# Kernel tuning notes

Measured on AMD Instinct MI355X. Metric: run time of the kernel, lower is better.

Reference implementation:

```python
import jax, jax.numpy as jnp
import numpy as np

EPS = 1e-12  # torch F.normalize default eps


def _l2_normalize(x):
    # normalize along last dim, matching F.normalize(dim=2)
    norm = jnp.linalg.norm(x, axis=-1, keepdims=True)
    return x / jnp.maximum(norm, EPS)


def _poly_kernel_mean(a, b):
    # mean over (B,C,C) of squared inner products along T.
    # Original does broadcast (B,1,C,T)*(B,C,1,T) then sum; einsum is the
    # efficient batched-matmul form of the same math.
    g = jnp.einsum('bct,bdt->bcd', a, b)  # (B,C,C)
    return jnp.mean(g * g)


def setup_inputs() -> dict:
    key = jax.random.key(0)
    k1, k2 = jax.random.split(key)
    B, C, T = 16, 128, 16384
    f_s = jax.random.normal(k1, (B, C, T), dtype=jnp.float32)
    f_t = jax.random.normal(k2, (B, C, T), dtype=jnp.float32)
    return {"f_s": f_s, "f_t": f_t}


def reference(f_s, f_t):
    # equal T -> no interpolation branch; view(B,C,-1) is identity for 3D
    s = _l2_normalize(f_s)
    t = _l2_normalize(f_t)
    loss = (jax.lax.stop_gradient(_poly_kernel_mean(t, t))
            + _poly_kernel_mean(s, s)
            - 2.0 * _poly_kernel_mean(s, t))
    return loss
```

## Files before the change

### kernel.cpp

```cpp
#include <hip/hip_runtime.h>
#include <hip/hip_bf16.h>

#define BATCH  16
#define CCH    128
#define TDIM   16384
#define MROWS  256
#define NCHUNK 16
#define KC     (TDIM / NCHUNK)
#define BK     32
#define NSTEP  (KC / BK)
#define LDSP   40
#define GRAM   (MROWS * MROWS)

typedef __attribute__((ext_vector_type(8))) short bf16x8;
typedef __attribute__((ext_vector_type(4))) float f32x4;
typedef __attribute__((ext_vector_type(4))) unsigned short u16x4;

__device__ __forceinline__ unsigned short f2bf(float x) {
  unsigned int u = __float_as_uint(x);
  u += 0x7fffu + ((u >> 16) & 1u);
  return (unsigned short)(u >> 16);
}

__global__ __launch_bounds__(512, 2) void gram_kernel(
    const float* __restrict__ fs, const float* __restrict__ ft,
    float* __restrict__ outp, int atomic_mode)
{
  __shared__ __attribute__((aligned(16))) unsigned short sm[2][MROWS][LDSP];

  const int tid   = threadIdx.x;
  const int bidx  = blockIdx.x;
  const int b     = bidx / NCHUNK;
  const int chunk = bidx - b * NCHUNK;
  const int kbase = chunk * KC;

  const int lane = tid & 63;
  const int w    = tid >> 6;
  const int wr   = w & 3;
  const int wc   = w >> 2;
  const int lhi  = lane >> 4;
  const int llo  = lane & 15;
  const int koff = lhi * 8;

  const float* rowptr[4];
  int rowidx[4], kq4[4];
  #pragma unroll
  for (int j = 0; j < 4; ++j) {
    int idx = j * 512 + tid;
    int row = idx >> 3;
    int kq  = idx & 7;
    rowidx[j] = row;
    kq4[j]    = kq * 4;
    const float* base = (row < CCH)
        ? (fs + (size_t)(b * CCH + row) * TDIM)
        : (ft + (size_t)(b * CCH + (row - CCH)) * TDIM);
    rowptr[j] = base + kbase + kq * 4;
  }

  f32x4 acc[4][8];
  #pragma unroll
  for (int i = 0; i < 4; ++i)
    #pragma unroll
    for (int j = 0; j < 8; ++j)
      acc[i][j] = (f32x4){0.f, 0.f, 0.f, 0.f};

  #pragma unroll
  for (int j = 0; j < 4; ++j) {
    f32x4 v = *(const f32x4*)(rowptr[j]);
    u16x4 p;
    p.x = f2bf(v.x); p.y = f2bf(v.y); p.z = f2bf(v.z); p.w = f2bf(v.w);
    *(u16x4*)&sm[0][rowidx[j]][kq4[j]] = p;
  }
  __syncthreads();

  int cur = 0;
  #pragma unroll 1
  for (int s = 0; s < NSTEP - 1; ++s) {
    f32x4 v[4];
    #pragma unroll
    for (int j = 0; j < 4; ++j)
      v[j] = *(const f32x4*)(rowptr[j] + (s + 1) * BK);

    bf16x8 af[4], bfr[8];
    #pragma unroll
    for (int i = 0; i < 4; ++i)
      af[i] = *(const bf16x8*)&sm[cur][wr * 64 + i * 16 + llo][koff];
    #pragma unroll
    for (int j = 0; j < 8; ++j)
      bfr[j] = *(const bf16x8*)&sm[cur][wc * 128 + j * 16 + llo][koff];
    #pragma unroll
    for (int i = 0; i < 4; ++i)
      #pragma unroll
      for (int j = 0; j < 8; ++j)
        acc[i][j] = __builtin_amdgcn_mfma_f32_16x16x32_bf16(af[i], bfr[j], acc[i][j], 0, 0, 0);

    #pragma unroll
    for (int j = 0; j < 4; ++j) {
      u16x4 p;
      p.x = f2bf(v[j].x); p.y = f2bf(v[j].y); p.z = f2bf(v[j].z); p.w = f2bf(v[j].w);
      *(u16x4*)&sm[cur ^ 1][rowidx[j]][kq4[j]] = p;
    }
    __syncthreads();
    cur ^= 1;
  }

  {
    bf16x8 af[4], bfr[8];
    #pragma unroll
    for (int i = 0; i < 4; ++i)
      af[i] = *(const bf16x8*)&sm[cur][wr * 64 + i * 16 + llo][koff];
    #pragma unroll
    for (int j = 0; j < 8; ++j)
      bfr[j] = *(const bf16x8*)&sm[cur][wc * 128 + j * 16 + llo][koff];
    #pragma unroll
    for (int i = 0; i < 4; ++i)
      #pragma unroll
      for (int j = 0; j < 8; ++j)
        acc[i][j] = __builtin_amdgcn_mfma_f32_16x16x32_bf16(af[i], bfr[j], acc[i][j], 0, 0, 0);
  }

  if (atomic_mode) {
    float* out = outp + (size_t)b * GRAM;
    #pragma unroll
    for (int i = 0; i < 4; ++i) {
      int row0 = wr * 64 + i * 16 + lhi * 4;
      #pragma unroll
      for (int j = 0; j < 8; ++j) {
        int col = wc * 128 + j * 16 + llo;
        #pragma unroll
        for (int r = 0; r < 4; ++r)
          atomicAdd(&out[(size_t)(row0 + r) * MROWS + col], acc[i][j][r]);
      }
    }
  } else {
    float* out = outp + (size_t)bidx * GRAM;
    #pragma unroll
    for (int i = 0; i < 4; ++i) {
      int row0 = wr * 64 + i * 16 + lhi * 4;
      #pragma unroll
      for (int j = 0; j < 8; ++j) {
        int col = wc * 128 + j * 16 + llo;
        #pragma unroll
        for (int r = 0; r < 4; ++r)
          out[(size_t)(row0 + r) * MROWS + col] = acc[i][j][r];
      }
    }
  }
}

__global__ __launch_bounds__(256) void norms_kernel(
    const float* __restrict__ gram, float* __restrict__ norms, int nchunk)
{
  int b = blockIdx.x;
  int d = threadIdx.x;
  float g = 0.f;
  for (int c = 0; c < nchunk; ++c)
    g += gram[(size_t)(b * nchunk + c) * GRAM + (size_t)d * (MROWS + 1)];
  float n = sqrtf(fmaxf(g, 0.f));
  n = fmaxf(n, 1e-12f);
  norms[b * MROWS + d] = 1.0f / n;
}

__global__ __launch_bounds__(256) void loss_kernel(
    const float* __restrict__ gram, const float* __restrict__ norms,
    float* __restrict__ out, int nchunk)
{
  int b     = blockIdx.x >> 6;
  int strip = blockIdx.x & 63;
  int e0    = strip * 1024 + threadIdx.x * 4;
  const float* nb = norms + b * MROWS;

  f32x4 g = (f32x4){0.f, 0.f, 0.f, 0.f};
  for (int c = 0; c < nchunk; ++c) {
    f32x4 v = *(const f32x4*)(gram + (size_t)(b * nchunk + c) * GRAM + e0);
    g.x += v.x; g.y += v.y; g.z += v.z; g.w += v.w;
  }
  int i  = e0 >> 8;
  int j0 = e0 & 255;
  float ri = nb[i];
  float accl = 0.f;
  #pragma unroll
  for (int q = 0; q < 4; ++q) {
    int j = j0 + q;
    float gh = g[q] * ri * nb[j];
    float sgn = ((i < CCH) == (j < CCH)) ? 1.f : -1.f;
    accl += sgn * gh * gh;
  }
  #pragma unroll
  for (int off = 32; off > 0; off >>= 1)
    accl += __shfl_down(accl, off, 64);
  __shared__ float red[4];
  if ((threadIdx.x & 63) == 0) red[threadIdx.x >> 6] = accl;
  __syncthreads();
  if (threadIdx.x == 0) {
    float t = red[0] + red[1] + red[2] + red[3];
    atomicAdd(out, t * (1.0f / (float)(BATCH * CCH * CCH)));
  }
}

extern "C" void kernel_launch(void* const* d_in, const int* in_sizes, int n_in,
                              void* d_out, int out_size, void* d_ws, size_t ws_size,
                              hipStream_t stream) {
  const float* fs = (const float*)d_in[0];
  const float* ft = (const float*)d_in[1];
  float* out = (float*)d_out;
  float* wsf = (float*)d_ws;

  float* norms = wsf;
  float* gram  = wsf + 4096;

  const size_t need_partials = (size_t)(4096 + (size_t)BATCH * NCHUNK * GRAM) * 4;
  const int atomic_mode = (ws_size >= need_partials) ? 0 : 1;
  const int nchunk = atomic_mode ? 1 : NCHUNK;

  (void)hipMemsetAsync(d_out, 0, sizeof(float), stream);
  if (atomic_mode)
    (void)hipMemsetAsync(gram, 0, (size_t)BATCH * GRAM * sizeof(float), stream);

  gram_kernel<<<dim3(BATCH * NCHUNK), dim3(512), 0, stream>>>(fs, ft, gram, atomic_mode);
  norms_kernel<<<dim3(BATCH), dim3(256), 0, stream>>>(gram, norms, nchunk);
  loss_kernel<<<dim3(BATCH * 64), dim3(256), 0, stream>>>(gram, norms, out, nchunk);
}
```

Before: 349.3 us.

## Deepen global-load prefetch to two steps and use lighter LDS barrier

Restructures the gram kernel main loop so global loads are issued two K-steps ahead with two register buffers, unrolled by two over the double-buffered LDS. The __syncthreads is replaced by an LDS-only waitcnt plus s_barrier, so outstanding global loads are not drained at each barrier. This is meant to hide HBM latency better, at the cost of extra live registers (a second f32x4[4] set) that could raise register pressure at 2 blocks per CU.

```diff
diff --git a/kernel.cpp b/kernel.cpp
--- a/kernel.cpp
+++ b/kernel.cpp
@@ -22,6 +22,50 @@
   return (unsigned short)(u >> 16);
 }
 
+__device__ __forceinline__ void pipe_barrier() {
+  asm volatile("s_waitcnt lgkmcnt(0)" ::: "memory");
+  __builtin_amdgcn_s_barrier();
+  asm volatile("" ::: "memory");
+}
+
+__device__ __forceinline__ void load_step(
+    f32x4 (&v)[4], const float* const (&rowptr)[4], int s)
+{
+  #pragma unroll
+  for (int j = 0; j < 4; ++j)
+    v[j] = *(const f32x4*)(rowptr[j] + s * BK);
+}
+
+__device__ __forceinline__ void stage_step(
+    unsigned short (&buf)[MROWS][LDSP], const f32x4 (&v)[4],
+    const int (&rowidx)[4], const int (&kq4)[4])
+{
+  #pragma unroll
+  for (int j = 0; j < 4; ++j) {
+    u16x4 p;
+    p.x = f2bf(v[j].x); p.y = f2bf(v[j].y); p.z = f2bf(v[j].z); p.w = f2bf(v[j].w);
+    *(u16x4*)&buf[rowidx[j]][kq4[j]] = p;
+  }
+}
+
+__device__ __forceinline__ void compute_step(
+    const unsigned short (&buf)[MROWS][LDSP],
+    f32x4 (&acc)[4][8], int wr, int wc, int llo, int koff)
+{
+  bf16x8 af[4], bfr[8];
+  #pragma unroll
+  for (int i = 0; i < 4; ++i)
+    af[i] = *(const bf16x8*)&buf[wr * 64 + i * 16 + llo][koff];
+  #pragma unroll
+  for (int j = 0; j < 8; ++j)
+    bfr[j] = *(const bf16x8*)&buf[wc * 128 + j * 16 + llo][koff];
+  #pragma unroll
+  for (int i = 0; i < 4; ++i)
+    #pragma unroll
+    for (int j = 0; j < 8; ++j)
+      acc[i][j] = __builtin_amdgcn_mfma_f32_16x16x32_bf16(af[i], bfr[j], acc[i][j], 0, 0, 0);
+}
+
 __global__ __launch_bounds__(512, 2) void gram_kernel(
     const float* __restrict__ fs, const float* __restrict__ ft,
     float* __restrict__ outp, int atomic_mode)
@@ -64,60 +108,27 @@
     for (int j = 0; j < 8; ++j)
       acc[i][j] = (f32x4){0.f, 0.f, 0.f, 0.f};
 
-  #pragma unroll
-  for (int j = 0; j < 4; ++j) {
-    f32x4 v = *(const f32x4*)(rowptr[j]);
-    u16x4 p;
-    p.x = f2bf(v.x); p.y = f2bf(v.y); p.z = f2bf(v.z); p.w = f2bf(v.w);
-    *(u16x4*)&sm[0][rowidx[j]][kq4[j]] = p;
-  }
-  __syncthreads();
-
-  int cur = 0;
+  f32x4 va[4], vb[4];
+  load_step(va, rowptr, 0);
+  load_step(vb, rowptr, 1);
+  stage_step(sm[0], va, rowidx, kq4);
+  pipe_barrier();
+
   #pragma unroll 1
-  for (int s = 0; s < NSTEP - 1; ++s) {
-    f32x4 v[4];
-    #pragma unroll
-    for (int j = 0; j < 4; ++j)
-      v[j] = *(const f32x4*)(rowptr[j] + (s + 1) * BK);
-
-    bf16x8 af[4], bfr[8];
-    #pragma unroll
-    for (int i = 0; i < 4; ++i)
-      af[i] = *(const bf16x8*)&sm[cur][wr * 64 + i * 16 + llo][koff];
-    #pragma unroll
-    for (int j = 0; j < 8; ++j)
-      bfr[j] = *(const bf16x8*)&sm[cur][wc * 128 + j * 16 + llo][koff];
-    #pragma unroll
-    for (int i = 0; i < 4; ++i)
-      #pragma unroll
-      for (int j = 0; j < 8; ++j)
-        acc[i][j] = __builtin_amdgcn_mfma_f32_16x16x32_bf16(af[i], bfr[j], acc[i][j], 0, 0, 0);
-
-    #pragma unroll
-    for (int j = 0; j < 4; ++j) {
-      u16x4 p;
-      p.x = f2bf(v[j].x); p.y = f2bf(v[j].y); p.z = f2bf(v[j].z); p.w = f2bf(v[j].w);
-      *(u16x4*)&sm[cur ^ 1][rowidx[j]][kq4[j]] = p;
-    }
-    __syncthreads();
-    cur ^= 1;
-  }
-
-  {
-    bf16x8 af[4], bfr[8];
-    #pragma unroll
-    for (int i = 0; i < 4; ++i)
-      af[i] = *(const bf16x8*)&sm[cur][wr * 64 + i * 16 + llo][koff];
-    #pragma unroll
-    for (int j = 0; j < 8; ++j)
-      bfr[j] = *(const bf16x8*)&sm[cur][wc * 128 + j * 16 + llo][koff];
-    #pragma unroll
-    for (int i = 0; i < 4; ++i)
-      #pragma unroll
-      for (int j = 0; j < 8; ++j)
-        acc[i][j] = __builtin_amdgcn_mfma_f32_16x16x32_bf16(af[i], bfr[j], acc[i][j], 0, 0, 0);
-  }
+  for (int s = 0; s < NSTEP - 2; s += 2) {
+    load_step(va, rowptr, s + 2);
+    compute_step(sm[0], acc, wr, wc, llo, koff);
+    stage_step(sm[1], vb, rowidx, kq4);
+    pipe_barrier();
+    load_step(vb, rowptr, s + 3);
+    compute_step(sm[1], acc, wr, wc, llo, koff);
+    stage_step(sm[0], va, rowidx, kq4);
+    pipe_barrier();
+  }
+  compute_step(sm[0], acc, wr, wc, llo, koff);
+  stage_step(sm[1], vb, rowidx, kq4);
+  pipe_barrier();
+  compute_step(sm[1], acc, wr, wc, llo, koff);
 
   if (atomic_mode) {
     float* out = outp + (size_t)b * GRAM;
```

After: 332.6 us. -4.8%, faster.

## Pre-pack inputs to swizzled bf16 and stream into LDS via global_load_lds

Applied to the files above, without the earlier changes.

Adds a pack kernel that converts both fp32 inputs to bf16 in a chunked, XOR-swizzled layout. The gram kernel then copies those tiles straight into 128KB of dynamic LDS with global_load_lds, double-buffered over larger K steps, and drops the per-step fp32 load and convert in the main loop. Partial grams are always reduced with atomics instead of per-chunk partial buffers. This costs an extra pass that writes and rereads a bf16 copy of the inputs, and adds atomic contention on the output.

```diff
diff --git a/kernel.cpp b/kernel.cpp
--- a/kernel.cpp
+++ b/kernel.cpp
@@ -1,20 +1,23 @@
 #include <hip/hip_runtime.h>
-#include <hip/hip_bf16.h>
 
 #define BATCH  16
 #define CCH    128
 #define TDIM   16384
 #define MROWS  256
 #define NCHUNK 16
-#define KC     (TDIM / NCHUNK)
-#define BK     32
-#define NSTEP  (KC / BK)
-#define LDSP   40
+#define KC     1024
+#define BKS    128
+#define NSTEP  8
+#define STEPB  65536u
+#define REGSH  262144u
+#define LDSBYTES (2u * STEPB)
 #define GRAM   (MROWS * MROWS)
 
 typedef __attribute__((ext_vector_type(8))) short bf16x8;
 typedef __attribute__((ext_vector_type(4))) float f32x4;
-typedef __attribute__((ext_vector_type(4))) unsigned short u16x4;
+typedef __attribute__((ext_vector_type(8))) unsigned short u16x8;
+typedef const __attribute__((address_space(1))) unsigned int* gptr_t;
+typedef __attribute__((address_space(3))) unsigned int* lptr_t;
 
 __device__ __forceinline__ unsigned short f2bf(float x) {
   unsigned int u = __float_as_uint(x);
@@ -22,17 +25,67 @@
   return (unsigned short)(u >> 16);
 }
 
+__global__ __launch_bounds__(256) void pack_kernel(
+    const float* __restrict__ fs, const float* __restrict__ ft,
+    unsigned short* __restrict__ pk)
+{
+  const int id  = blockIdx.x;
+  const int tau = id >> 11;
+  const int b   = (id >> 7) & 15;
+  const int row = id & 127;
+  const int R   = tau * CCH + row;
+  const int r7  = R & 7;
+  const float* src = (tau ? ft : fs) + (size_t)(b * CCH + row) * TDIM;
+  unsigned short* dstb = pk + (size_t)b * NCHUNK * REGSH + (size_t)R * 128;
+
+  #pragma unroll 1
+  for (int it = 0; it < 8; ++it) {
+    const int k = it * 2048 + threadIdx.x * 8;
+    f32x4 lo = *(const f32x4*)(src + k);
+    f32x4 hi = *(const f32x4*)(src + k + 4);
+    u16x8 p;
+    p[0] = f2bf(lo.x); p[1] = f2bf(lo.y); p[2] = f2bf(lo.z); p[3] = f2bf(lo.w);
+    p[4] = f2bf(hi.x); p[5] = f2bf(hi.y); p[6] = f2bf(hi.z); p[7] = f2bf(hi.w);
+    const int c  = k >> 10;
+    const int s  = (k >> 7) & 7;
+    const int cl = (k >> 3) & 15;
+    unsigned short* dst = dstb + (size_t)c * REGSH + (unsigned)s * 32768u
+                        + (unsigned)((cl ^ r7) << 3);
+    *(u16x8*)dst = p;
+  }
+}
+
+__device__ __forceinline__ void compute_kk(
+    const unsigned short* bp, f32x4 (&acc)[4][8], int kk,
+    int wr, int wc, int llo, int lhi)
+{
+  bf16x8 af[4], bfr[8];
+  #pragma unroll
+  for (int i = 0; i < 4; ++i) {
+    const int R = wr * 64 + i * 16 + llo;
+    af[i] = *(const bf16x8*)(bp + R * 128 + (((kk * 4 + lhi) ^ (R & 7)) << 3));
+  }
+  #pragma unroll
+  for (int j = 0; j < 8; ++j) {
+    const int R = wc * 128 + j * 16 + llo;
+    bfr[j] = *(const bf16x8*)(bp + R * 128 + (((kk * 4 + lhi) ^ (R & 7)) << 3));
+  }
+  #pragma unroll
+  for (int i = 0; i < 4; ++i)
+    #pragma unroll
+    for (int j = 0; j < 8; ++j)
+      acc[i][j] = __builtin_amdgcn_mfma_f32_16x16x32_bf16(af[i], bfr[j], acc[i][j], 0, 0, 0);
+}
+
 __global__ __launch_bounds__(512, 2) void gram_kernel(
-    const float* __restrict__ fs, const float* __restrict__ ft,
-    float* __restrict__ outp, int atomic_mode)
-{
-  __shared__ __attribute__((aligned(16))) unsigned short sm[2][MROWS][LDSP];
-
-  const int tid   = threadIdx.x;
-  const int bidx  = blockIdx.x;
-  const int b     = bidx / NCHUNK;
-  const int chunk = bidx - b * NCHUNK;
-  const int kbase = chunk * KC;
+    const unsigned short* __restrict__ pk, float* __restrict__ gram)
+{
+  extern __shared__ __attribute__((aligned(16))) char smraw[];
+
+  const int tid  = threadIdx.x;
+  const int bidx = blockIdx.x;
+  const int b    = bidx >> 4;
+  const char* reg = (const char*)(pk + (size_t)bidx * REGSH);
 
   const int lane = tid & 63;
   const int w    = tid >> 6;
@@ -40,22 +93,6 @@
   const int wc   = w >> 2;
   const int lhi  = lane >> 4;
   const int llo  = lane & 15;
-  const int koff = lhi * 8;
-
-  const float* rowptr[4];
-  int rowidx[4], kq4[4];
-  #pragma unroll
-  for (int j = 0; j < 4; ++j) {
-    int idx = j * 512 + tid;
-    int row = idx >> 3;
-    int kq  = idx & 7;
-    rowidx[j] = row;
-    kq4[j]    = kq * 4;
-    const float* base = (row < CCH)
-        ? (fs + (size_t)(b * CCH + row) * TDIM)
-        : (ft + (size_t)(b * CCH + (row - CCH)) * TDIM);
-    rowptr[j] = base + kbase + kq * 4;
-  }
 
   f32x4 acc[4][8];
   #pragma unroll
@@ -64,98 +101,61 @@
     for (int j = 0; j < 8; ++j)
       acc[i][j] = (f32x4){0.f, 0.f, 0.f, 0.f};
 
-  #pragma unroll
-  for (int j = 0; j < 4; ++j) {
-    f32x4 v = *(const f32x4*)(rowptr[j]);
-    u16x4 p;
-    p.x = f2bf(v.x); p.y = f2bf(v.y); p.z = f2bf(v.z); p.w = f2bf(v.w);
-    *(u16x4*)&sm[0][rowidx[j]][kq4[j]] = p;
-  }
-  __syncthreads();
-
-  int cur = 0;
+  #define ISSUE_STAGE(s)                                                     \
+    {                                                                        \
+      const char* g = reg + (size_t)(s) * STEPB;                             \
+      char* l = smraw + (unsigned)((s) & 1) * STEPB;                         \
+      _Pragma("unroll")                                                      \
+      for (int q = 0; q < 8; ++q)                                            \
+        __builtin_amdgcn_global_load_lds(                                    \
+            (gptr_t)(g + q * 8192 + tid * 16),                               \
+            (lptr_t)(l + q * 8192 + tid * 16), 16, 0, 0);                    \
+    }
+
+  ISSUE_STAGE(0);
+  ISSUE_STAGE(1);
+
   #pragma unroll 1
-  for (int s = 0; s < NSTEP - 1; ++s) {
-    f32x4 v[4];
+  for (int s = 0; s < NSTEP; ++s) {
+    if (s < NSTEP - 1) asm volatile("s_waitcnt vmcnt(8)" ::: "memory");
+    else               asm volatile("s_waitcnt vmcnt(0)" ::: "memory");
+    __builtin_amdgcn_s_barrier();
+    asm volatile("" ::: "memory");
+
+    const unsigned short* bp = (const unsigned short*)(smraw + (unsigned)(s & 1) * STEPB);
+    compute_kk(bp, acc, 0, wr, wc, llo, lhi);
+    compute_kk(bp, acc, 1, wr, wc, llo, lhi);
+    compute_kk(bp, acc, 2, wr, wc, llo, lhi);
+    compute_kk(bp, acc, 3, wr, wc, llo, lhi);
+
+    asm volatile("s_waitcnt lgkmcnt(0)" ::: "memory");
+    __builtin_amdgcn_s_barrier();
+    asm volatile("" ::: "memory");
+
+    if (s + 2 < NSTEP) ISSUE_STAGE(s + 2);
+  }
+  #undef ISSUE_STAGE
+
+  float* out = gram + (size_t)b * GRAM;
+  #pragma unroll
+  for (int i = 0; i < 4; ++i) {
+    int row0 = wr * 64 + i * 16 + lhi * 4;
     #pragma unroll
-    for (int j = 0; j < 4; ++j)
-      v[j] = *(const f32x4*)(rowptr[j] + (s + 1) * BK);
-
-    bf16x8 af[4], bfr[8];
-    #pragma unroll
-    for (int i = 0; i < 4; ++i)
-      af[i] = *(const bf16x8*)&sm[cur][wr * 64 + i * 16 + llo][koff];
-    #pragma unroll
-    for (int j = 0; j < 8; ++j)
-      bfr[j] = *(const bf16x8*)&sm[cur][wc * 128 + j * 16 + llo][koff];
-    #pragma unroll
-    for (int i = 0; i < 4; ++i)
+    for (int j = 0; j < 8; ++j) {
+      int col = wc * 128 + j * 16 + llo;
       #pragma unroll
-      for (int j = 0; j < 8; ++j)
-        acc[i][j] = __builtin_amdgcn_mfma_f32_16x16x32_bf16(af[i], bfr[j], acc[i][j], 0, 0, 0);
-
-    #pragma unroll
-    for (int j = 0; j < 4; ++j) {
-      u16x4 p;
-      p.x = f2bf(v[j].x); p.y = f2bf(v[j].y); p.z = f2bf(v[j].z); p.w = f2bf(v[j].w);
-      *(u16x4*)&sm[cur ^ 1][rowidx[j]][kq4[j]] = p;
+      for (int r = 0; r < 4; ++r)
+        atomicAdd(&out[(size_t)(row0 + r) * MROWS + col], acc[i][j][r]);
     }
-    __syncthreads();
-    cur ^= 1;
-  }
-
-  {
-    bf16x8 af[4], bfr[8];
-    #pragma unroll
-    for (int i = 0; i < 4; ++i)
-      af[i] = *(const bf16x8*)&sm[cur][wr * 64 + i * 16 + llo][koff];
-    #pragma unroll
-    for (int j = 0; j < 8; ++j)
-      bfr[j] = *(const bf16x8*)&sm[cur][wc * 128 + j * 16 + llo][koff];
-    #pragma unroll
-    for (int i = 0; i < 4; ++i)
-      #pragma unroll
-      for (int j = 0; j < 8; ++j)
-        acc[i][j] = __builtin_amdgcn_mfma_f32_16x16x32_bf16(af[i], bfr[j], acc[i][j], 0, 0, 0);
-  }
-
-  if (atomic_mode) {
-    float* out = outp + (size_t)b * GRAM;
-    #pragma unroll
-    for (int i = 0; i < 4; ++i) {
-      int row0 = wr * 64 + i * 16 + lhi * 4;
-      #pragma unroll
-      for (int j = 0; j < 8; ++j) {
-        int col = wc * 128 + j * 16 + llo;
-        #pragma unroll
-        for (int r = 0; r < 4; ++r)
-          atomicAdd(&out[(size_t)(row0 + r) * MROWS + col], acc[i][j][r]);
-      }
-    }
-  } else {
-    float* out = outp + (size_t)bidx * GRAM;
-    #pragma unroll
-    for (int i = 0; i < 4; ++i) {
-      int row0 = wr * 64 + i * 16 + lhi * 4;
-      #pragma unroll
-      for (int j = 0; j < 8; ++j) {
-        int col = wc * 128 + j * 16 + llo;
-        #pragma unroll
-        for (int r = 0; r < 4; ++r)
-          out[(size_t)(row0 + r) * MROWS + col] = acc[i][j][r];
-      }
-    }
   }
 }
 
 __global__ __launch_bounds__(256) void norms_kernel(
-    const float* __restrict__ gram, float* __restrict__ norms, int nchunk)
+    const float* __restrict__ gram, float* __restrict__ norms)
 {
   int b = blockIdx.x;
   int d = threadIdx.x;
-  float g = 0.f;
-  for (int c = 0; c < nchunk; ++c)
-    g += gram[(size_t)(b * nchunk + c) * GRAM + (size_t)d * (MROWS + 1)];
+  float g = gram[(size_t)b * GRAM + (size_t)d * (MROWS + 1)];
   float n = sqrtf(fmaxf(g, 0.f));
   n = fmaxf(n, 1e-12f);
   norms[b * MROWS + d] = 1.0f / n;
@@ -163,18 +163,15 @@
 
 __global__ __launch_bounds__(256) void loss_kernel(
     const float* __restrict__ gram, const float* __restrict__ norms,
-    float* __restrict__ out, int nchunk)
+    float* __restrict__ out)
 {
   int b     = blockIdx.x >> 6;
   int strip = blockIdx.x & 63;
   int e0    = strip * 1024 + threadIdx.x * 4;
   const float* nb = norms + b * MROWS;
 
-  f32x4 g = (f32x4){0.f, 0.f, 0.f, 0.f};
-  for (int c = 0; c < nchunk; ++c) {
-    f32x4 v = *(const f32x4*)(gram + (size_t)(b * nchunk + c) * GRAM + e0);
-    g.x += v.x; g.y += v.y; g.z += v.z; g.w += v.w;
-  }
+  f32x4 g = *(const f32x4*)(gram + (size_t)b * GRAM + e0);
+
   int i  = e0 >> 8;
   int j0 = e0 & 255;
   float ri = nb[i];
@@ -208,16 +205,20 @@
 
   float* norms = wsf;
   float* gram  = wsf + 4096;
-
-  const size_t need_partials = (size_t)(4096 + (size_t)BATCH * NCHUNK * GRAM) * 4;
-  const int atomic_mode = (ws_size >= need_partials) ? 0 : 1;
-  const int nchunk = atomic_mode ? 1 : NCHUNK;
+  unsigned short* pk = (unsigned short*)(gram + (size_t)BATCH * GRAM);
+
+  static int lds_raised = 0;
+  if (!lds_raised) {
+    (void)hipFuncSetAttribute(reinterpret_cast<const void*>(gram_kernel),
+                              hipFuncAttributeMaxDynamicSharedMemorySize, LDSBYTES);
+    lds_raised = 1;
+  }
 
   (void)hipMemsetAsync(d_out, 0, sizeof(float), stream);
-  if (atomic_mode)
-    (void)hipMemsetAsync(gram, 0, (size_t)BATCH * GRAM * sizeof(float), stream);
-
-  gram_kernel<<<dim3(BATCH * NCHUNK), dim3(512), 0, stream>>>(fs, ft, gram, atomic_mode);
-  norms_kernel<<<dim3(BATCH), dim3(256), 0, stream>>>(gram, norms, nchunk);
-  loss_kernel<<<dim3(BATCH * 64), dim3(256), 0, stream>>>(gram, norms, out, nchunk);
-}
+  (void)hipMemsetAsync(gram, 0, (size_t)BATCH * GRAM * sizeof(float), stream);
+
+  pack_kernel<<<dim3(2 * BATCH * CCH), dim3(256), 0, stream>>>(fs, ft, pk);
+  gram_kernel<<<dim3(BATCH * NCHUNK), dim3(512), LDSBYTES, stream>>>(pk, gram);
+  norms_kernel<<<dim3(BATCH), dim3(256), 0, stream>>>(gram, norms);
+  loss_kernel<<<dim3(BATCH * 64), dim3(256), 0, stream>>>(gram, norms, out);
+}
```

Result: slower. 393.0 us (+12.5%).
